# Performance work log

Hardware: AMD Instinct MI355X
Metric: run time of the kernel (lower is better)

Reference implementation:

```python
import jax, jax.numpy as jnp
import numpy as np

N_NODES = 50000
N_EDGES = 800000
D_FEAT = 64


def setup_inputs() -> dict:
    key = jax.random.key(0)
    k1, k2, k3 = jax.random.split(key, 3)
    x_sum = jax.random.normal(k1, (N_NODES, D_FEAT), dtype=jnp.float32)
    x_prod = jax.random.uniform(k2, (N_NODES, D_FEAT), dtype=jnp.float32)
    edge_index = jax.random.randint(k3, (2, N_EDGES), 0, N_NODES, dtype=jnp.int64)
    return {"x_sum": x_sum, "x_prod": x_prod, "edge_index": edge_index}


def reference(x_sum, x_prod, edge_index):
    # flow='source_to_target' -> gather from edge_index[0], aggregate at edge_index[1]
    src_idx = edge_index[0]
    dst_idx = edge_index[1]
    n = x_sum.shape[0]

    # __lift__: index_select along node dim (message is identity; edge_attr/norm None)
    m_sum = x_sum[src_idx]    # [E, D]
    m_prod = x_prod[src_idx]  # [E, D]

    # scatter_sum: zeros-init + scatter_add_
    out_sum = jax.ops.segment_sum(m_sum, dst_idx, num_segments=n)

    # scatter_product: ones-init + scatter_(reduce='multiply')
    out_prod = jnp.ones((n, x_prod.shape[1]), dtype=x_prod.dtype).at[dst_idx].multiply(m_prod)

    return out_sum, out_prod
```

## Files before the change

kernel.cpp:

```cpp
#include <hip/hip_runtime.h>
#include <hip/hip_fp16.h>

#define N_NODES 50000
#define N_EDGES 800000
#define D_FEAT  64
#define BSHIFT  6
#define NBKT    782
#define NB      64
#define CHUNK   12500
#define PSHIFT  20
#define SRC_MASK ((1 << PSHIFT) - 1)

#define WS_FLAG    0
#define WS_TOT     64
#define WS_COFF    (WS_TOT + NBKT)
#define WS_BH      (WS_COFF + NBKT + 1)
#define WS_OFFS    (WS_BH + NB * NBKT)
#define WS_PAIR    (WS_OFFS + N_NODES + 1)
#define WS_SSRC    (WS_PAIR + N_EDGES)
#define WS_PACKED  (WS_SSRC + N_EDGES)
#define WS_INTS    (WS_PACKED + N_NODES * D_FEAT)

__device__ inline void detect_idx_layout(const int* idx, int* flag) {
    int allzero = 1;
    #pragma unroll
    for (int i = 1; i < 129; i += 2) {
        if (idx[i] != 0) allzero = 0;
    }
    *flag = allzero;
}

__global__ __launch_bounds__(256) void init_cast(int* __restrict__ W,
                                                 const int* __restrict__ idx,
                                                 const float* __restrict__ xs,
                                                 const float* __restrict__ xp) {
    int tid = blockIdx.x * blockDim.x + threadIdx.x;
    int stride = gridDim.x * blockDim.x;
    __half2* packed = (__half2*)(W + WS_PACKED);
    const int total = N_NODES * D_FEAT;
    for (int i = tid; i < total; i += stride)
        packed[i] = __floats2half2_rn(xs[i], xp[i]);
    if (tid == 0) {
        detect_idx_layout(idx, W + WS_FLAG);
        W[WS_OFFS + N_NODES] = N_EDGES;
    }
}

__global__ __launch_bounds__(256) void block_hist(const int* __restrict__ idx,
                                                  int* __restrict__ W) {
    __shared__ int h[NBKT];
    for (int i = threadIdx.x; i < NBKT; i += 256) h[i] = 0;
    __syncthreads();
    const int flg = W[WS_FLAG];
    const int base = blockIdx.x * CHUNK;
    for (int e = base + threadIdx.x; e < base + CHUNK; e += 256) {
        int dst = flg ? idx[2 * (N_EDGES + e)] : idx[N_EDGES + e];
        atomicAdd(&h[dst >> BSHIFT], 1);
    }
    __syncthreads();
    for (int i = threadIdx.x; i < NBKT; i += 256)
        W[WS_BH + blockIdx.x * NBKT + i] = h[i];
}

__global__ __launch_bounds__(64) void bucket_scan(int* __restrict__ W) {
    int j = blockIdx.x;
    int l = threadIdx.x;
    int c = W[WS_BH + l * NBKT + j];
    int incl = c;
    #pragma unroll
    for (int off = 1; off < 64; off <<= 1) {
        int u = __shfl_up(incl, off, 64);
        if (l >= off) incl += u;
    }
    W[WS_BH + l * NBKT + j] = incl - c;
    if (l == 63) W[WS_TOT + j] = incl;
}

__global__ __launch_bounds__(1024) void base_scan(int* __restrict__ W) {
    __shared__ int part[1024];
    int t = threadIdx.x;
    int v = (t < NBKT) ? W[WS_TOT + t] : 0;
    part[t] = v;
    __syncthreads();
    for (int off = 1; off < 1024; off <<= 1) {
        int u = (t >= off) ? part[t - off] : 0;
        __syncthreads();
        part[t] += u;
        __syncthreads();
    }
    if (t < NBKT) W[WS_COFF + t] = part[t] - v;
    if (t == 0) W[WS_COFF + NBKT] = N_EDGES;
}

__global__ __launch_bounds__(256) void coarse_scatter(const int* __restrict__ idx,
                                                      int* __restrict__ W) {
    __shared__ int cur[NBKT];
    for (int i = threadIdx.x; i < NBKT; i += 256)
        cur[i] = W[WS_COFF + i] + W[WS_BH + blockIdx.x * NBKT + i];
    __syncthreads();
    const int flg = W[WS_FLAG];
    const int base = blockIdx.x * CHUNK;
    for (int e = base + threadIdx.x; e < base + CHUNK; e += 256) {
        int src, dst;
        if (flg) { src = idx[2 * e]; dst = idx[2 * (N_EDGES + e)]; }
        else     { src = idx[e];     dst = idx[N_EDGES + e]; }
        int pos = atomicAdd(&cur[dst >> BSHIFT], 1);
        W[WS_PAIR + pos] = src | ((dst & 63) << PSHIFT);
    }
}

__global__ __launch_bounds__(256) void fine_sort(int* __restrict__ W) {
    __shared__ int h[64];
    int b = blockIdx.x;
    int t = threadIdx.x;
    int bbase = W[WS_COFF + b];
    int bend  = W[WS_COFF + b + 1];
    if (t < 64) h[t] = 0;
    __syncthreads();
    for (int e = bbase + t; e < bend; e += 256)
        atomicAdd(&h[(unsigned)W[WS_PAIR + e] >> PSHIFT], 1);
    __syncthreads();
    if (t < 64) {
        int c = h[t];
        int incl = c;
        #pragma unroll
        for (int off = 1; off < 64; off <<= 1) {
            int u = __shfl_up(incl, off, 64);
            if (t >= off) incl += u;
        }
        int excl = incl - c;
        int node = (b << BSHIFT) + t;
        if (node < N_NODES) W[WS_OFFS + node] = bbase + excl;
        h[t] = excl;
    }
    __syncthreads();
    for (int e = bbase + t; e < bend; e += 256) {
        int v = W[WS_PAIR + e];
        int p = atomicAdd(&h[(unsigned)v >> PSHIFT], 1);
        W[WS_SSRC + bbase + p] = v & SRC_MASK;
    }
}

__global__ __launch_bounds__(256) void gather_reduce(const int* __restrict__ W,
                                                     float* __restrict__ out) {
    int wave = (int)((blockIdx.x * blockDim.x + threadIdx.x) >> 6);
    int lane = threadIdx.x & 63;
    if (wave >= N_NODES) return;
    int beg = W[WS_OFFS + wave];
    int end = W[WS_OFFS + wave + 1];
    const int* ssrc = W + WS_SSRC;
    const __half2* packed = (const __half2*)(W + WS_PACKED);

    float s0 = 0.f, s1 = 0.f, s2 = 0.f, s3 = 0.f;
    float p0 = 1.f, p1 = 1.f, p2 = 1.f, p3 = 1.f;
    int i = beg;
    for (; i + 3 < end; i += 4) {
        int a = ssrc[i], b = ssrc[i + 1], c = ssrc[i + 2], d = ssrc[i + 3];
        float2 fa = __half22float2(packed[a * D_FEAT + lane]);
        float2 fb = __half22float2(packed[b * D_FEAT + lane]);
        float2 fc = __half22float2(packed[c * D_FEAT + lane]);
        float2 fd = __half22float2(packed[d * D_FEAT + lane]);
        s0 += fa.x; s1 += fb.x; s2 += fc.x; s3 += fd.x;
        p0 *= fa.y; p1 *= fb.y; p2 *= fc.y; p3 *= fd.y;
    }
    for (; i < end; ++i) {
        float2 f = __half22float2(packed[ssrc[i] * D_FEAT + lane]);
        s0 += f.x;
        p0 *= f.y;
    }
    out[(long)wave * D_FEAT + lane] = (s0 + s1) + (s2 + s3);
    out[(long)N_NODES * D_FEAT + (long)wave * D_FEAT + lane] = (p0 * p1) * (p2 * p3);
}

__device__ inline void atomicMulF32(float* addr, float val) {
    unsigned int* ua = (unsigned int*)addr;
    unsigned int old = __hip_atomic_load(ua, __ATOMIC_RELAXED, __HIP_MEMORY_SCOPE_AGENT);
    while (true) {
        unsigned int assumed = old;
        unsigned int desired = __float_as_uint(__uint_as_float(assumed) * val);
        old = atomicCAS(ua, assumed, desired);
        if (old == assumed) break;
    }
}

__global__ void fb_init(float* __restrict__ out, int* __restrict__ flag,
                        const int* __restrict__ idx) {
    const int n4 = (N_NODES * D_FEAT) / 4;
    int tid = blockIdx.x * blockDim.x + threadIdx.x;
    int stride = gridDim.x * blockDim.x;
    float4* o = (float4*)out;
    const float4 z = make_float4(0.f, 0.f, 0.f, 0.f);
    const float4 one = make_float4(1.f, 1.f, 1.f, 1.f);
    for (int i = tid; i < n4; i += stride) { o[i] = z; o[n4 + i] = one; }
    if (blockIdx.x == 0 && threadIdx.x == 0) detect_idx_layout(idx, flag);
}

__global__ void fb_scatter(const float* __restrict__ xs, const float* __restrict__ xp,
                           const int* __restrict__ idx, float* __restrict__ out,
                           const int* __restrict__ flag) {
    long tid = (long)blockIdx.x * blockDim.x + threadIdx.x;
    const long total = (long)N_EDGES * (D_FEAT / 4);
    if (tid >= total) return;
    int e = (int)(tid >> 4);
    int c = (int)(tid & 15);
    int src, dst;
    if (*flag) { src = idx[2 * e]; dst = idx[2 * (N_EDGES + e)]; }
    else       { src = idx[e];     dst = idx[N_EDGES + e]; }
    const float4 s = ((const float4*)(xs + (long)src * D_FEAT))[c];
    const float4 p = ((const float4*)(xp + (long)src * D_FEAT))[c];
    float* os = out + (long)dst * D_FEAT + c * 4;
    float* op = out + (long)N_NODES * D_FEAT + (long)dst * D_FEAT + c * 4;
    atomicAdd(os + 0, s.x); atomicAdd(os + 1, s.y);
    atomicAdd(os + 2, s.z); atomicAdd(os + 3, s.w);
    atomicMulF32(op + 0, p.x); atomicMulF32(op + 1, p.y);
    atomicMulF32(op + 2, p.z); atomicMulF32(op + 3, p.w);
}

extern "C" void kernel_launch(void* const* d_in, const int* in_sizes, int n_in,
                              void* d_out, int out_size, void* d_ws, size_t ws_size,
                              hipStream_t stream) {
    const float* x_sum  = (const float*)d_in[0];
    const float* x_prod = (const float*)d_in[1];
    const int*   eidx   = (const int*)d_in[2];
    float* out = (float*)d_out;
    int* W = (int*)d_ws;

    if (ws_size < (size_t)WS_INTS * sizeof(int)) {
        fb_init<<<1024, 256, 0, stream>>>(out, W, eidx);
        const long total = (long)N_EDGES * (D_FEAT / 4);
        int grid = (int)((total + 255) / 256);
        fb_scatter<<<grid, 256, 0, stream>>>(x_sum, x_prod, eidx, out, W);
        return;
    }

    init_cast<<<1024, 256, 0, stream>>>(W, eidx, x_sum, x_prod);
    block_hist<<<NB, 256, 0, stream>>>(eidx, W);
    bucket_scan<<<NBKT, 64, 0, stream>>>(W);
    base_scan<<<1, 1024, 0, stream>>>(W);
    coarse_scatter<<<NB, 256, 0, stream>>>(eidx, W);
    fine_sort<<<NBKT, 256, 0, stream>>>(W);
    gather_reduce<<<(N_NODES + 3) / 4, 256, 0, stream>>>(W, out);
}
```

Baseline: 171.3 us.

## Widen histogram/scatter grid to 256 blocks, transpose bucket histogram, unroll gather by 8

Raises the number of blocks in the histogram and coarse scatter passes from 64 to 256, so those passes occupy more compute units with smaller chunks. The per-block bucket histogram is stored bucket-major, and the bucket scan becomes a 256-thread shared-memory scan. The gather-reduce loop is unrolled to 8 independent gathers with a readfirstlane on the segment bounds, to expose more memory-level parallelism. The costs are a larger histogram workspace and a slower synchronised scan per bucket.

```diff
diff --git a/kernel.cpp b/kernel.cpp
--- a/kernel.cpp
+++ b/kernel.cpp
@@ -6,8 +6,8 @@
 #define D_FEAT  64
 #define BSHIFT  6
 #define NBKT    782
-#define NB      64
-#define CHUNK   12500
+#define NB      256
+#define CHUNK   3125
 #define PSHIFT  20
 #define SRC_MASK ((1 << PSHIFT) - 1)
 
@@ -15,7 +15,7 @@
 #define WS_TOT     64
 #define WS_COFF    (WS_TOT + NBKT)
 #define WS_BH      (WS_COFF + NBKT + 1)
-#define WS_OFFS    (WS_BH + NB * NBKT)
+#define WS_OFFS    (WS_BH + NBKT * NB)
 #define WS_PAIR    (WS_OFFS + N_NODES + 1)
 #define WS_SSRC    (WS_PAIR + N_EDGES)
 #define WS_PACKED  (WS_SSRC + N_EDGES)
@@ -59,21 +59,24 @@
     }
     __syncthreads();
     for (int i = threadIdx.x; i < NBKT; i += 256)
-        W[WS_BH + blockIdx.x * NBKT + i] = h[i];
-}
-
-__global__ __launch_bounds__(64) void bucket_scan(int* __restrict__ W) {
+        W[WS_BH + i * NB + blockIdx.x] = h[i];
+}
+
+__global__ __launch_bounds__(256) void bucket_scan(int* __restrict__ W) {
+    __shared__ int part[NB];
     int j = blockIdx.x;
-    int l = threadIdx.x;
-    int c = W[WS_BH + l * NBKT + j];
-    int incl = c;
-    #pragma unroll
-    for (int off = 1; off < 64; off <<= 1) {
-        int u = __shfl_up(incl, off, 64);
-        if (l >= off) incl += u;
-    }
-    W[WS_BH + l * NBKT + j] = incl - c;
-    if (l == 63) W[WS_TOT + j] = incl;
+    int t = threadIdx.x;
+    int c = W[WS_BH + j * NB + t];
+    part[t] = c;
+    __syncthreads();
+    for (int off = 1; off < NB; off <<= 1) {
+        int u = (t >= off) ? part[t - off] : 0;
+        __syncthreads();
+        part[t] += u;
+        __syncthreads();
+    }
+    W[WS_BH + j * NB + t] = part[t] - c;
+    if (t == NB - 1) W[WS_TOT + j] = part[t];
 }
 
 __global__ __launch_bounds__(1024) void base_scan(int* __restrict__ W) {
@@ -96,7 +99,7 @@
                                                       int* __restrict__ W) {
     __shared__ int cur[NBKT];
     for (int i = threadIdx.x; i < NBKT; i += 256)
-        cur[i] = W[WS_COFF + i] + W[WS_BH + blockIdx.x * NBKT + i];
+        cur[i] = W[WS_COFF + i] + W[WS_BH + i * NB + blockIdx.x];
     __syncthreads();
     const int flg = W[WS_FLAG];
     const int base = blockIdx.x * CHUNK;
@@ -146,30 +149,48 @@
     int wave = (int)((blockIdx.x * blockDim.x + threadIdx.x) >> 6);
     int lane = threadIdx.x & 63;
     if (wave >= N_NODES) return;
-    int beg = W[WS_OFFS + wave];
-    int end = W[WS_OFFS + wave + 1];
+    int beg = __builtin_amdgcn_readfirstlane(W[WS_OFFS + wave]);
+    int end = __builtin_amdgcn_readfirstlane(W[WS_OFFS + wave + 1]);
     const int* ssrc = W + WS_SSRC;
     const __half2* packed = (const __half2*)(W + WS_PACKED);
 
     float s0 = 0.f, s1 = 0.f, s2 = 0.f, s3 = 0.f;
+    float s4 = 0.f, s5 = 0.f, s6 = 0.f, s7 = 0.f;
     float p0 = 1.f, p1 = 1.f, p2 = 1.f, p3 = 1.f;
+    float p4 = 1.f, p5 = 1.f, p6 = 1.f, p7 = 1.f;
     int i = beg;
-    for (; i + 3 < end; i += 4) {
-        int a = ssrc[i], b = ssrc[i + 1], c = ssrc[i + 2], d = ssrc[i + 3];
-        float2 fa = __half22float2(packed[a * D_FEAT + lane]);
-        float2 fb = __half22float2(packed[b * D_FEAT + lane]);
-        float2 fc = __half22float2(packed[c * D_FEAT + lane]);
-        float2 fd = __half22float2(packed[d * D_FEAT + lane]);
-        s0 += fa.x; s1 += fb.x; s2 += fc.x; s3 += fd.x;
-        p0 *= fa.y; p1 *= fb.y; p2 *= fc.y; p3 *= fd.y;
-    }
-    for (; i < end; ++i) {
+    for (; i + 7 < end; i += 8) {
+        int a0 = ssrc[i],     a1 = ssrc[i + 1], a2 = ssrc[i + 2], a3 = ssrc[i + 3];
+        int a4 = ssrc[i + 4], a5 = ssrc[i + 5], a6 = ssrc[i + 6], a7 = ssrc[i + 7];
+        float2 f0 = __half22float2(packed[a0 * D_FEAT + lane]);
+        float2 f1 = __half22float2(packed[a1 * D_FEAT + lane]);
+        float2 f2 = __half22float2(packed[a2 * D_FEAT + lane]);
+        float2 f3 = __half22float2(packed[a3 * D_FEAT + lane]);
+        float2 f4 = __half22float2(packed[a4 * D_FEAT + lane]);
+        float2 f5 = __half22float2(packed[a5 * D_FEAT + lane]);
+        float2 f6 = __half22float2(packed[a6 * D_FEAT + lane]);
+        float2 f7 = __half22float2(packed[a7 * D_FEAT + lane]);
+        s0 += f0.x; s1 += f1.x; s2 += f2.x; s3 += f3.x;
+        s4 += f4.x; s5 += f5.x; s6 += f6.x; s7 += f7.x;
+        p0 *= f0.y; p1 *= f1.y; p2 *= f2.y; p3 *= f3.y;
+        p4 *= f4.y; p5 *= f5.y; p6 *= f6.y; p7 *= f7.y;
+    }
+    for (; i + 1 < end; i += 2) {
+        int a0 = ssrc[i], a1 = ssrc[i + 1];
+        float2 f0 = __half22float2(packed[a0 * D_FEAT + lane]);
+        float2 f1 = __half22float2(packed[a1 * D_FEAT + lane]);
+        s0 += f0.x; s1 += f1.x;
+        p0 *= f0.y; p1 *= f1.y;
+    }
+    if (i < end) {
         float2 f = __half22float2(packed[ssrc[i] * D_FEAT + lane]);
         s0 += f.x;
         p0 *= f.y;
     }
-    out[(long)wave * D_FEAT + lane] = (s0 + s1) + (s2 + s3);
-    out[(long)N_NODES * D_FEAT + (long)wave * D_FEAT + lane] = (p0 * p1) * (p2 * p3);
+    float ssum = ((s0 + s1) + (s2 + s3)) + ((s4 + s5) + (s6 + s7));
+    float pprd = ((p0 * p1) * (p2 * p3)) * ((p4 * p5) * (p6 * p7));
+    out[(long)wave * D_FEAT + lane] = ssum;
+    out[(long)N_NODES * D_FEAT + (long)wave * D_FEAT + lane] = pprd;
 }
 
 __device__ inline void atomicMulF32(float* addr, float val) {
@@ -235,7 +256,7 @@
 
     init_cast<<<1024, 256, 0, stream>>>(W, eidx, x_sum, x_prod);
     block_hist<<<NB, 256, 0, stream>>>(eidx, W);
-    bucket_scan<<<NBKT, 64, 0, stream>>>(W);
+    bucket_scan<<<NBKT, 256, 0, stream>>>(W);
     base_scan<<<1, 1024, 0, stream>>>(W);
     coarse_scatter<<<NB, 256, 0, stream>>>(eidx, W);
     fine_sort<<<NBKT, 256, 0, stream>>>(W);
```

Result: faster. 148.2 us (-13.5%).
